# Kernel tuning notes

Measured on AMD Instinct MI355X. Metric: run time of the kernel, lower is better.

## Reference

```python
import jax, jax.numpy as jnp
import numpy as np
from jax import lax

B, T, S = 64, 4096, 64


def setup_inputs() -> dict:
    key = jax.random.key(0)
    k1, k2, k3 = jax.random.split(key, 3)
    transition_potentials = jax.random.normal(k1, (S, S), dtype=jnp.float32)
    emission_potentials = jax.random.normal(k2, (B, T, S), dtype=jnp.float32)
    seq_lens = jax.random.randint(k3, (B,), 1, T + 1)
    return {
        "transition_potentials": transition_potentials,
        "emission_potentials": emission_potentials,
        "seq_lens": seq_lens,
    }


def reference(transition_potentials, emission_potentials, seq_lens):
    # potential_normalization='none', potential_scale=1.0 -> normalize is identity.
    # HMM forward algorithm: alpha[t] = logsumexp_i(alpha[t-1,i] + A[i,j]) + emis[t]
    alpha0 = emission_potentials[:, 0, :]  # [B,S]

    def step(alpha_prev, emis_t):
        # alpha_prev: [B,S]; emis_t: [B,S]; transition: [S,S]
        alpha_t = jax.nn.logsumexp(
            alpha_prev[:, :, None] + transition_potentials[None, :, :], axis=1
        ) + emis_t
        return alpha_t, alpha_t

    emis_rest = jnp.moveaxis(emission_potentials[:, 1:, :], 1, 0)  # [T-1,B,S]
    _, alphas = lax.scan(step, alpha0, emis_rest)  # [T-1,B,S]
    alpha = jnp.concatenate([alpha0[None], alphas], axis=0)  # [T,B,S]
    alpha = jnp.moveaxis(alpha, 0, 1)  # [B,T,S]
    log_Z = jax.nn.logsumexp(alpha[:, -1, :], axis=-1)  # [B]
    return alpha, log_Z
```

## Files before the change

kernel.cpp:

```cpp
#include <hip/hip_runtime.h>
#include <hip/hip_bf16.h>


#define BB 64
#define TT 4096
#define SS 64
#define C_CH 128
#define LL 32
#define WARM 24
#define PF 8

typedef __attribute__((ext_vector_type(4))) short bh4;
typedef __attribute__((ext_vector_type(4))) float f32x4;

#define LOG2E 1.44269504088896340736f
#define LN2F  0.69314718055994530942f

__device__ __forceinline__ float fexp2(float x) {
#if __has_builtin(__builtin_amdgcn_exp2f)
    return __builtin_amdgcn_exp2f(x);
#else
    return exp2f(x);
#endif
}
__device__ __forceinline__ float flog2(float x) {
#if __has_builtin(__builtin_amdgcn_logf)
    return __builtin_amdgcn_logf(x);
#else
    return log2f(x);
#endif
}
__device__ __forceinline__ int pack_bf16(float x, float y) {
    __hip_bfloat162 h = __float22bfloat162_rn(make_float2(x, y));
    int r; __builtin_memcpy(&r, &h, 4); return r;
}
union PB2 { int i[2]; bh4 v; };

__device__ __forceinline__ f32x4 mfma16(bh4 a, bh4 b, f32x4 c) {
#if __has_builtin(__builtin_amdgcn_mfma_f32_16x16x16bf16_1k)
    return __builtin_amdgcn_mfma_f32_16x16x16bf16_1k(a, b, c, 0, 0, 0);
#else
    asm("v_mfma_f32_16x16x16_bf16 %0, %1, %2, %0" : "+v"(c) : "v"(a), "v"(b));
    return c;
#endif
}

__device__ __forceinline__ void do_step(f32x4 (&vv)[4], const f32x4 (&eE)[4],
                                        const bh4 (&Af)[4][4]) {
    bh4 Bf[4];
    #pragma unroll
    for (int kb = 0; kb < 4; ++kb) {
        PB2 pb;
        pb.i[0] = pack_bf16(vv[kb].x, vv[kb].y);
        pb.i[1] = pack_bf16(vv[kb].z, vv[kb].w);
        Bf[kb] = pb.v;
    }
    #pragma unroll
    for (int jt = 0; jt < 4; ++jt) {
        f32x4 d0 = {0.f, 0.f, 0.f, 0.f};
        f32x4 d1 = {0.f, 0.f, 0.f, 0.f};
        d0 = mfma16(Af[jt][0], Bf[0], d0);
        d1 = mfma16(Af[jt][1], Bf[1], d1);
        d0 = mfma16(Af[jt][2], Bf[2], d0);
        d1 = mfma16(Af[jt][3], Bf[3], d1);
        f32x4 d = d0 + d1;
        vv[jt] = d * eE[jt];
    }
}

__device__ __forceinline__ void load_row(f32x4 (&dst)[4],
                                         const float* __restrict__ eb,
                                         int t, int off) {
    const float* p = eb + (t & (TT - 1)) * SS + off;
    #pragma unroll
    for (int jt = 0; jt < 4; ++jt)
        dst[jt] = *(const f32x4*)(p + 16 * jt);
}

__global__ __launch_bounds__(64)
__attribute__((amdgpu_waves_per_eu(1, 1)))
void hmm_phaseA(const float* __restrict__ trans,
                const float* __restrict__ emis,
                float* __restrict__ out,
                float* __restrict__ ws_warm,
                float* __restrict__ ws_bound) {
    const int lane = threadIdx.x;
    const int n = lane & 15, q = lane >> 4;
    const int w = blockIdx.x;
    const int b = w >> 3, cg = w & 7;
    const int c = 16 * cg + n;
    const bool is_c0 = (c == 0);
    const int off = 4 * q;

    bh4 Af[4][4];
    #pragma unroll
    for (int jt = 0; jt < 4; ++jt)
        #pragma unroll
        for (int kb = 0; kb < 4; ++kb) {
            float v0 = __expf(trans[(16 * kb + 4 * q + 0) * SS + 16 * jt + n]) * 0.015625f;
            float v1 = __expf(trans[(16 * kb + 4 * q + 1) * SS + 16 * jt + n]) * 0.015625f;
            float v2 = __expf(trans[(16 * kb + 4 * q + 2) * SS + 16 * jt + n]) * 0.015625f;
            float v3 = __expf(trans[(16 * kb + 4 * q + 3) * SS + 16 * jt + n]) * 0.015625f;
            PB2 pb;
            pb.i[0] = pack_bf16(v0, v1);
            pb.i[1] = pack_bf16(v2, v3);
            Af[jt][kb] = pb.v;
        }

    const float* eb = emis + (size_t)b * TT * SS;
    float*       ob = out  + (size_t)b * TT * SS;

    const int t0 = LL * c - (WARM + 1);

    const float cL = is_c0 ? (-150.0f * LN2F) : 0.0f;

    f32x4 vv[4], e0v[4], ebuf[PF][4];
    {
        f32x4 a0[4], z0[4];
        load_row(a0, eb, t0, off);
        load_row(z0, eb, 0, off);
        #pragma unroll
        for (int jt = 0; jt < 4; ++jt) {
            vv[jt].x = fexp2(a0[jt].x * LOG2E);
            vv[jt].y = fexp2(a0[jt].y * LOG2E);
            vv[jt].z = fexp2(a0[jt].z * LOG2E);
            vv[jt].w = fexp2(a0[jt].w * LOG2E);
            e0v[jt].x = fexp2(z0[jt].x * LOG2E);
            e0v[jt].y = fexp2(z0[jt].y * LOG2E);
            e0v[jt].z = fexp2(z0[jt].z * LOG2E);
            e0v[jt].w = fexp2(z0[jt].w * LOG2E);
        }
    }
    #pragma unroll
    for (int k = 0; k < PF; ++k) load_row(ebuf[k], eb, t0 + 1 + k, off);

    #pragma unroll 1
    for (int g = 0; g < 3; ++g) {
        #pragma unroll
        for (int k = 0; k < PF; ++k) {
            int s = PF * g + k + 1;
            f32x4 eE[4];
            #pragma unroll
            for (int jt = 0; jt < 4; ++jt) {
                eE[jt].x = fexp2(ebuf[k][jt].x * LOG2E);
                eE[jt].y = fexp2(ebuf[k][jt].y * LOG2E);
                eE[jt].z = fexp2(ebuf[k][jt].z * LOG2E);
                eE[jt].w = fexp2(ebuf[k][jt].w * LOG2E);
            }
            load_row(ebuf[k], eb, t0 + s + PF, off);
            do_step(vv, eE, Af);
        }
    }
    if (lane < 16)
        ws_warm[b * C_CH + 16 * cg + lane] =
            fmaf(flog2(vv[0].x), LN2F, 144.0f * LN2F + cL);

    #pragma unroll 1
    for (int g = 0; g < 4; ++g) {
        #pragma unroll
        for (int k = 0; k < PF; ++k) {
            int s = WARM + 1 + PF * g + k;
            f32x4 eE[4];
            #pragma unroll
            for (int jt = 0; jt < 4; ++jt) {
                eE[jt].x = fexp2(ebuf[k][jt].x * LOG2E);
                eE[jt].y = fexp2(ebuf[k][jt].y * LOG2E);
                eE[jt].z = fexp2(ebuf[k][jt].z * LOG2E);
                eE[jt].w = fexp2(ebuf[k][jt].w * LOG2E);
            }
            load_row(ebuf[k], eb, t0 + s + PF, off);
            do_step(vv, eE, Af);
            if (k == 0 && g == 0 && is_c0) {
                #pragma unroll
                for (int jt = 0; jt < 4; ++jt) vv[jt] = e0v[jt];
            }
            const float cs = 6.0f * (float)s * LN2F + cL;
            float* p = ob + (t0 + s) * SS + off;
            #pragma unroll
            for (int jt = 0; jt < 4; ++jt) {
                f32x4 a;
                a.x = fmaf(flog2(vv[jt].x), LN2F, cs);
                a.y = fmaf(flog2(vv[jt].y), LN2F, cs);
                a.z = fmaf(flog2(vv[jt].z), LN2F, cs);
                a.w = fmaf(flog2(vv[jt].w), LN2F, cs);
                *(f32x4*)(p + 16 * jt) = a;
            }
        }
    }
    if (lane < 16)
        ws_bound[b * C_CH + 16 * cg + lane] =
            fmaf(flog2(vv[0].x), LN2F, 336.0f * LN2F + cL);
}

__global__ __launch_bounds__(256)
void hmm_phaseC(float* __restrict__ out,
                const float* __restrict__ ws_warm,
                const float* __restrict__ ws_bound) {
    const int b = blockIdx.x, c = blockIdx.y, tid = threadIdx.x;
    __shared__ float sd[C_CH];

    if (tid < C_CH) {
        float d = 0.f;
        if (tid > 0)
            d = ws_bound[b * C_CH + tid - 1] - ws_warm[b * C_CH + tid];
        sd[tid] = d;
    }
    __syncthreads();
    #pragma unroll
    for (int off = 1; off < C_CH; off <<= 1) {
        float v = 0.f;
        if (tid >= off && tid < C_CH) v = sd[tid - off];
        __syncthreads();
        if (tid >= off && tid < C_CH) sd[tid] += v;
        __syncthreads();
    }
    const float delta = sd[c];

    float4* p4 = (float4*)(out + (size_t)b * TT * SS + (size_t)c * LL * SS);
    float4 last;
    #pragma unroll
    for (int i = 0; i < 2; ++i) {
        int idx = tid + 256 * i;
        float4 v = p4[idx];
        v.x += delta; v.y += delta; v.z += delta; v.w += delta;
        p4[idx] = v;
        last = v;
    }

    if (c == C_CH - 1 && tid >= 240) {
        float mx = fmaxf(fmaxf(last.x, last.y), fmaxf(last.z, last.w));
        #pragma unroll
        for (int off = 8; off >= 1; off >>= 1)
            mx = fmaxf(mx, __shfl_xor(mx, off, 64));
        float sv = __expf(last.x - mx) + __expf(last.y - mx)
                 + __expf(last.z - mx) + __expf(last.w - mx);
        #pragma unroll
        for (int off = 8; off >= 1; off >>= 1)
            sv += __shfl_xor(sv, off, 64);
        if (tid == 240)
            out[(size_t)BB * TT * SS + b] = mx + __logf(sv);
    }
}

extern "C" void kernel_launch(void* const* d_in, const int* in_sizes, int n_in,
                              void* d_out, int out_size, void* d_ws, size_t ws_size,
                              hipStream_t stream) {
    const float* trans = (const float*)d_in[0];
    const float* emis  = (const float*)d_in[1];
    float* out = (float*)d_out;

    float* ws_warm  = (float*)d_ws;
    float* ws_bound = ws_warm + BB * C_CH;

    hmm_phaseA<<<dim3(BB * 8), dim3(64), 0, stream>>>(trans, emis, out,
                                                      ws_warm, ws_bound);
    hmm_phaseC<<<dim3(BB, C_CH), dim3(256), 0, stream>>>(out, ws_warm, ws_bound);
}
```

Measured before the change: 153.5 us.

## Stash bf16 linear alphas in workspace and defer log conversion to fixup kernel

Phase A no longer takes logs and writes fp32 alphas straight to the output. It stores the raw linear-domain alpha values as bf16 into a per-wave workspace slab. Phase C then reads the bf16 values, applies log2, the per-step scale constant and the prefix delta, and writes the fp32 output once. This removes the read-modify-write of the full output in phase C and moves the log work off the serial recurrence. In exchange, stored alphas are rounded to bf16 before the log, which costs accuracy.

```diff
diff --git a/kernel.cpp b/kernel.cpp
--- a/kernel.cpp
+++ b/kernel.cpp
@@ -9,9 +9,11 @@
 #define LL 32
 #define WARM 24
 #define PF 8
+#define WSLAB 32768
 
 typedef __attribute__((ext_vector_type(4))) short bh4;
 typedef __attribute__((ext_vector_type(4))) float f32x4;
+typedef __attribute__((ext_vector_type(4))) unsigned short us4;
 
 #define LOG2E 1.44269504088896340736f
 #define LN2F  0.69314718055994530942f
@@ -34,7 +36,11 @@
     __hip_bfloat162 h = __float22bfloat162_rn(make_float2(x, y));
     int r; __builtin_memcpy(&r, &h, 4); return r;
 }
-union PB2 { int i[2]; bh4 v; };
+__device__ __forceinline__ float bf_to_f32(unsigned short u) {
+    unsigned int w = ((unsigned int)u) << 16;
+    float f; __builtin_memcpy(&f, &w, 4); return f;
+}
+union PB2 { int i[2]; bh4 v; us4 u; };
 
 __device__ __forceinline__ f32x4 mfma16(bh4 a, bh4 b, f32x4 c) {
 #if __has_builtin(__builtin_amdgcn_mfma_f32_16x16x16bf16_1k)
@@ -81,7 +87,7 @@
 __attribute__((amdgpu_waves_per_eu(1, 1)))
 void hmm_phaseA(const float* __restrict__ trans,
                 const float* __restrict__ emis,
-                float* __restrict__ out,
+                unsigned short* __restrict__ wsv,
                 float* __restrict__ ws_warm,
                 float* __restrict__ ws_bound) {
     const int lane = threadIdx.x;
@@ -108,7 +114,7 @@
         }
 
     const float* eb = emis + (size_t)b * TT * SS;
-    float*       ob = out  + (size_t)b * TT * SS;
+    unsigned short* wslab = wsv + (size_t)w * WSLAB;
 
     const int t0 = LL * c - (WARM + 1);
 
@@ -174,16 +180,13 @@
                 #pragma unroll
                 for (int jt = 0; jt < 4; ++jt) vv[jt] = e0v[jt];
             }
-            const float cs = 6.0f * (float)s * LN2F + cL;
-            float* p = ob + (t0 + s) * SS + off;
+            unsigned short* wp = wslab + (n * 32 + (s - (WARM + 1))) * 64 + 4 * q;
             #pragma unroll
-            for (int jt = 0; jt < 4; ++jt) {
-                f32x4 a;
-                a.x = fmaf(flog2(vv[jt].x), LN2F, cs);
-                a.y = fmaf(flog2(vv[jt].y), LN2F, cs);
-                a.z = fmaf(flog2(vv[jt].z), LN2F, cs);
-                a.w = fmaf(flog2(vv[jt].w), LN2F, cs);
-                *(f32x4*)(p + 16 * jt) = a;
+            for (int kb = 0; kb < 4; ++kb) {
+                PB2 pb;
+                pb.i[0] = pack_bf16(vv[kb].x, vv[kb].y);
+                pb.i[1] = pack_bf16(vv[kb].z, vv[kb].w);
+                *(us4*)(wp + 16 * kb) = pb.u;
             }
         }
     }
@@ -194,6 +197,7 @@
 
 __global__ __launch_bounds__(256)
 void hmm_phaseC(float* __restrict__ out,
+                const unsigned short* __restrict__ wsv,
                 const float* __restrict__ ws_warm,
                 const float* __restrict__ ws_bound) {
     const int b = blockIdx.x, c = blockIdx.y, tid = threadIdx.x;
@@ -216,28 +220,41 @@
     }
     const float delta = sd[c];
 
-    float4* p4 = (float4*)(out + (size_t)b * TT * SS + (size_t)c * LL * SS);
-    float4 last;
-    #pragma unroll
-    for (int i = 0; i < 2; ++i) {
-        int idx = tid + 256 * i;
-        float4 v = p4[idx];
-        v.x += delta; v.y += delta; v.z += delta; v.w += delta;
-        p4[idx] = v;
-        last = v;
-    }
-
-    if (c == C_CH - 1 && tid >= 240) {
-        float mx = fmaxf(fmaxf(last.x, last.y), fmaxf(last.z, last.w));
-        #pragma unroll
-        for (int off = 8; off >= 1; off >>= 1)
+    const int cg = c >> 4, n = c & 15;
+    const unsigned short* src =
+        wsv + (size_t)(b * 8 + cg) * WSLAB + n * 2048 + tid * 8;
+    const int r = tid >> 3, col0 = (tid & 7) * 8;
+
+    us4 u0 = *(const us4*)(src);
+    us4 u1 = *(const us4*)(src + 4);
+
+    const float cs = fmaf(6.0f * (float)(r + 25), LN2F,
+                          (c == 0 ? -150.0f * LN2F : 0.0f) + delta);
+    float a[8];
+    #pragma unroll
+    for (int i = 0; i < 4; ++i) {
+        a[i]     = fmaf(flog2(bf_to_f32(u0[i])), LN2F, cs);
+        a[4 + i] = fmaf(flog2(bf_to_f32(u1[i])), LN2F, cs);
+    }
+
+    float* dst = out + (size_t)b * TT * SS + (size_t)(32 * c + r) * SS + col0;
+    *(f32x4*)(dst)     = *(f32x4*)&a[0];
+    *(f32x4*)(dst + 4) = *(f32x4*)&a[4];
+
+    if (c == C_CH - 1 && tid >= 248) {
+        float mx = a[0];
+        #pragma unroll
+        for (int i = 1; i < 8; ++i) mx = fmaxf(mx, a[i]);
+        #pragma unroll
+        for (int off = 4; off >= 1; off >>= 1)
             mx = fmaxf(mx, __shfl_xor(mx, off, 64));
-        float sv = __expf(last.x - mx) + __expf(last.y - mx)
-                 + __expf(last.z - mx) + __expf(last.w - mx);
-        #pragma unroll
-        for (int off = 8; off >= 1; off >>= 1)
+        float sv = 0.f;
+        #pragma unroll
+        for (int i = 0; i < 8; ++i) sv += __expf(a[i] - mx);
+        #pragma unroll
+        for (int off = 4; off >= 1; off >>= 1)
             sv += __shfl_xor(sv, off, 64);
-        if (tid == 240)
+        if (tid == 248)
             out[(size_t)BB * TT * SS + b] = mx + __logf(sv);
     }
 }
@@ -251,8 +268,11 @@
 
     float* ws_warm  = (float*)d_ws;
     float* ws_bound = ws_warm + BB * C_CH;
-
-    hmm_phaseA<<<dim3(BB * 8), dim3(64), 0, stream>>>(trans, emis, out,
+    unsigned short* wsv =
+        (unsigned short*)(ws_bound + BB * C_CH);
+
+    hmm_phaseA<<<dim3(BB * 8), dim3(64), 0, stream>>>(trans, emis, wsv,
                                                       ws_warm, ws_bound);
-    hmm_phaseC<<<dim3(BB, C_CH), dim3(256), 0, stream>>>(out, ws_warm, ws_bound);
-}
+    hmm_phaseC<<<dim3(BB, C_CH), dim3(256), 0, stream>>>(out, wsv,
+                                                         ws_warm, ws_bound);
+}
```

Measured after the change: 146.2 us. -4.7%, faster.
